# Optimization experiments

Measured on AMD Instinct MI355X. Metric: run time of the kernel, lower is better.

The kernel has to match this reference:

```python
import jax, jax.numpy as jnp
import numpy as np
import math

N, M = 512, 31
INP, EMB, ATT = 64, 64, 64
NUM_RELS = 200
SELF_LOOP_IDX = NUM_RELS  # index num_rels is the self-loop relation


def setup_inputs() -> dict:
    key = jax.random.key(0)
    ks = jax.random.split(key, 11)
    s_w = 1.0 / math.sqrt(EMB)
    return {
        "h": jax.random.normal(ks[0], (N, INP), jnp.float32),
        "msg": jax.random.normal(ks[1], (N, M, EMB), jnp.float32),
        "msg_type": jax.random.randint(ks[2], (N, M), 0, NUM_RELS, jnp.int32),
        "r_label_node": jax.random.randint(ks[3], (N,), 0, NUM_RELS, jnp.int32),
        "r_label_msg": jax.random.randint(ks[4], (N, M), 0, NUM_RELS, jnp.int32),
        "W_self": jax.random.normal(ks[5], (INP, EMB), jnp.float32) * s_w,
        "Q": jax.random.normal(ks[6], (NUM_RELS + 1, EMB, ATT), jnp.float32) * s_w,
        "K": jax.random.normal(ks[7], (NUM_RELS + 1, EMB, ATT), jnp.float32) * s_w,
        "V": jax.random.normal(ks[8], (NUM_RELS + 1, EMB, ATT), jnp.float32) * s_w,
        "ffn_w": jax.random.normal(ks[9], (ATT, EMB), jnp.float32) * s_w,
        "ffn_b": jnp.zeros((EMB,), jnp.float32),
    }


def reference(h, msg, msg_type, r_label_node, r_label_msg, W_self, Q, K, V, ffn_w, ffn_b):
    curr = h @ W_self                                        # [N, EMB]
    x = jnp.concatenate([curr[:, None, :], msg], axis=1)     # [N, M+1, EMB]
    qv_idx = jnp.concatenate([r_label_node[:, None], r_label_msg], axis=1)  # [N, M+1]
    self_col = jnp.full((x.shape[0], 1), SELF_LOOP_IDX, msg_type.dtype)
    k_idx = jnp.concatenate([self_col, msg_type], axis=1)    # [N, M+1]
    # relation-indexed per-token projection weights (irregular gather)
    q = jnp.einsum("nme,nmea->nma", x, Q[qv_idx])            # [N, M+1, ATT]
    k = jnp.einsum("nme,nmea->nma", x, K[k_idx])             # [N, M+1, ATT]
    v = jnp.einsum("nme,nmea->nma", x, V[qv_idx])            # [N, M+1, ATT]
    scores = jnp.einsum("nqa,nka->nqk", q, k) / math.sqrt(ATT)
    # NOTE: original code applies softmax over dim=1 (the query axis)
    att = jax.nn.softmax(scores, axis=1)                     # [N, M+1, M+1]
    pooled = jnp.einsum("nqk,nka->nqa", att, v)[:, 0]        # [N, ATT]
    return pooled @ ffn_w + ffn_b                            # [N, EMB]
```

## Files before the change

kernel.cpp:

```cpp
#include <hip/hip_runtime.h>
#include <math.h>

#define NN 512
#define MM 31
#define TT 32
#define EE 64
#define NREL 200
#define SELF_LOOP 200
#define QCAP 192
#define NT 6
#define WSTR 72
#define CPAD 32

typedef short  short8 __attribute__((ext_vector_type(8)));
typedef float  f32x4  __attribute__((ext_vector_type(4)));

__device__ __forceinline__ unsigned short f2bf(float f) {
    union { float f; unsigned int u; } a; a.f = f;
    unsigned int r = a.u + 0x7FFFu + ((a.u >> 16) & 1u);
    return (unsigned short)(r >> 16);
}

__global__ __launch_bounds__(64) void prep_scan_kernel(
    const float* __restrict__ h, const float* __restrict__ W_self,
    const float* __restrict__ K,
    const int* __restrict__ msg_type, const int* __restrict__ r_label_node,
    const int* __restrict__ r_label_msg,
    int* __restrict__ cnt_q, int* __restrict__ cnt_k,
    int* __restrict__ list_q, int* __restrict__ list_k,
    float* __restrict__ curr_all, float* __restrict__ k_all)
{
    const int n = blockIdx.x, a = threadIdx.x;

    if (a == 0) {
        int r = r_label_node[n];
        int p = atomicAdd(&cnt_q[r * CPAD], 1);
        if (p < QCAP) list_q[r * QCAP + p] = n * TT;
    }
    if (a < MM) {
        int j  = n * MM + a;
        int rl = r_label_msg[j];
        int p  = atomicAdd(&cnt_q[rl * CPAD], 1);
        if (p < QCAP) list_q[rl * QCAP + p] = n * TT + a + 1;
        int mt = msg_type[j];
        int p2 = atomicAdd(&cnt_k[mt * CPAD], 1);
        if (p2 < QCAP) list_k[mt * QCAP + p2] = n * TT + a + 1;
    }

    __shared__ float c_s[EE];
    const float* hrow = h + n * EE;
    float acc = 0.f;
#pragma unroll 8
    for (int e = 0; e < EE; ++e)
        acc = fmaf(hrow[e], W_self[e * EE + a], acc);
    curr_all[n * EE + a] = acc;
    c_s[a] = acc;
    __syncthreads();

    const float* K200 = K + (size_t)SELF_LOOP * EE * EE;
    float k0 = 0.f;
#pragma unroll 8
    for (int e = 0; e < EE; ++e)
        k0 = fmaf(c_s[e], K200[e * EE + a], k0);
    k_all[(size_t)n * TT * EE + a] = k0;
}

__global__ __launch_bounds__(256) void proj_tile_kernel(
    const float* __restrict__ curr_all, const float* __restrict__ msg,
    const float* __restrict__ Q, const float* __restrict__ K,
    const float* __restrict__ V,
    const int* __restrict__ cnt_q, const int* __restrict__ cnt_k,
    const int* __restrict__ list_q, const int* __restrict__ list_k,
    float* __restrict__ q_all, float* __restrict__ k_all,
    float* __restrict__ v_all)
{
    const int r    = blockIdx.x / NT;
    const int tile = blockIdx.x % NT;
    const int tid  = threadIdx.x;
    const int lane = tid & 63;
    const int wave = tid >> 6;
    const int col  = lane & 15;
    const int quad = lane >> 4;

    const int nq = min(cnt_q[r * CPAD], QCAP);
    const int nk = min(cnt_k[r * CPAD], QCAP);
    const int q0 = tile * 32;
    const bool do_q = q0 < nq;
    const bool do_k = q0 < nk;
    if (!do_q && !do_k) return;

    __shared__ unsigned short wq_s[EE * WSTR];
    __shared__ unsigned short wk_s[EE * WSTR];
    __shared__ unsigned short wv_s[EE * WSTR];
    __shared__ unsigned short x_s[64 * WSTR];
    __shared__ int tq_s[32], tk_s[32];

    {
        const int a = tid & 63, g = tid >> 6;
        if (do_q) {
            const float* Qp = Q + (size_t)r * EE * EE;
            const float* Vp = V + (size_t)r * EE * EE;
            unsigned short bq[16], bv[16];
#pragma unroll
            for (int j = 0; j < 16; ++j) {
                int e = g * 16 + j;
                bq[j] = f2bf(Qp[e * EE + a]);
                bv[j] = f2bf(Vp[e * EE + a]);
            }
            unsigned short* dq = &wq_s[a * WSTR + g * 16];
            unsigned short* dv = &wv_s[a * WSTR + g * 16];
            *(short8*)dq = *(short8*)&bq[0]; *(short8*)(dq + 8) = *(short8*)&bq[8];
            *(short8*)dv = *(short8*)&bv[0]; *(short8*)(dv + 8) = *(short8*)&bv[8];
        }
        if (do_k) {
            const float* Kp = K + (size_t)r * EE * EE;
            unsigned short bk[16];
#pragma unroll
            for (int j = 0; j < 16; ++j) {
                int e = g * 16 + j;
                bk[j] = f2bf(Kp[e * EE + a]);
            }
            unsigned short* dk = &wk_s[a * WSTR + g * 16];
            *(short8*)dk = *(short8*)&bk[0]; *(short8*)(dk + 8) = *(short8*)&bk[8];
        }
    }

    if (tid < 32) {
        tq_s[tid] = (do_q && q0 + tid < nq) ? list_q[r * QCAP + q0 + tid] : -1;
    } else if (tid < 64) {
        int i = tid - 32;
        tk_s[i] = (do_k && q0 + i < nk) ? list_k[r * QCAP + q0 + i] : -1;
    }

    {
        const int row = tid >> 2;
        const int fo  = (tid & 3) * 4;
        const bool qside = row < 32;
        const int li = qside ? (q0 + row) : (q0 + row - 32);
        const bool valid = qside ? (do_q && li < nq) : (do_k && li < nk);
        if (valid) {
            int token = qside ? list_q[r * QCAP + li] : list_k[r * QCAP + li];
            int n = token >> 5, t = token & 31;
            const float* src = (t == 0)
                ? (curr_all + n * EE)
                : (msg + ((size_t)n * MM + (t - 1)) * EE);
            float4 f0 = ((const float4*)src)[fo + 0];
            float4 f1 = ((const float4*)src)[fo + 1];
            float4 f2 = ((const float4*)src)[fo + 2];
            float4 f3 = ((const float4*)src)[fo + 3];
            unsigned short b[16] = {
                f2bf(f0.x), f2bf(f0.y), f2bf(f0.z), f2bf(f0.w),
                f2bf(f1.x), f2bf(f1.y), f2bf(f1.z), f2bf(f1.w),
                f2bf(f2.x), f2bf(f2.y), f2bf(f2.z), f2bf(f2.w),
                f2bf(f3.x), f2bf(f3.y), f2bf(f3.z), f2bf(f3.w) };
            unsigned short* d = &x_s[row * WSTR + fo * 4];
            *(short8*)d       = *(short8*)&b[0];
            *(short8*)(d + 8) = *(short8*)&b[8];
        }
    }
    __syncthreads();

    if (do_q) {
        const int mtile = wave & 1;
        const unsigned short* w_s = (wave >> 1) ? wv_s : wq_s;
        float* outp = (wave >> 1) ? v_all : q_all;
        const int m = mtile * 16 + col;
        f32x4 acc[4] = {{0,0,0,0},{0,0,0,0},{0,0,0,0},{0,0,0,0}};
#pragma unroll
        for (int kk = 0; kk < 2; ++kk) {
            short8 af = *(const short8*)&x_s[m * WSTR + kk * 32 + quad * 8];
#pragma unroll
            for (int nt = 0; nt < 4; ++nt) {
                short8 bf = *(const short8*)&w_s[(nt * 16 + col) * WSTR + kk * 32 + quad * 8];
                acc[nt] = __builtin_amdgcn_mfma_f32_16x16x32_bf16(af, bf, acc[nt], 0, 0, 0);
            }
        }
#pragma unroll
        for (int nt = 0; nt < 4; ++nt)
#pragma unroll
            for (int reg = 0; reg < 4; ++reg) {
                int rrow = mtile * 16 + quad * 4 + reg;
                int token = tq_s[rrow];
                if (token >= 0)
                    outp[(size_t)token * EE + nt * 16 + col] = acc[nt][reg];
            }
    }

    if (do_k) {
        const int mtile = wave & 1;
        const int nh = wave >> 1;
        const int m = 32 + mtile * 16 + col;
        f32x4 acc[2] = {{0,0,0,0},{0,0,0,0}};
#pragma unroll
        for (int kk = 0; kk < 2; ++kk) {
            short8 af = *(const short8*)&x_s[m * WSTR + kk * 32 + quad * 8];
#pragma unroll
            for (int j = 0; j < 2; ++j) {
                int nt = nh * 2 + j;
                short8 bf = *(const short8*)&wk_s[(nt * 16 + col) * WSTR + kk * 32 + quad * 8];
                acc[j] = __builtin_amdgcn_mfma_f32_16x16x32_bf16(af, bf, acc[j], 0, 0, 0);
            }
        }
#pragma unroll
        for (int j = 0; j < 2; ++j)
#pragma unroll
            for (int reg = 0; reg < 4; ++reg) {
                int rrow = mtile * 16 + quad * 4 + reg;
                int token = tk_s[rrow];
                if (token >= 0)
                    k_all[(size_t)token * EE + (nh * 2 + j) * 16 + col] = acc[j][reg];
            }
    }
}

__global__ __launch_bounds__(256) void attn_kernel(
    const float* __restrict__ q_all, const float* __restrict__ k_all,
    const float* __restrict__ v_all, const float* __restrict__ ffn_w,
    const float* __restrict__ ffn_b, float* __restrict__ out)
{
    const int n = blockIdx.x, tid = threadIdx.x;
    __shared__ float q_s[TT][68], k_s[TT][68], v_s[TT][68];
    __shared__ float s_s[TT][TT + 1];
    __shared__ float att0[TT];
    __shared__ float pooled[EE];

    {
        const float4* qg = (const float4*)(q_all + (size_t)n * TT * EE);
        const float4* kg = (const float4*)(k_all + (size_t)n * TT * EE);
        const float4* vg = (const float4*)(v_all + (size_t)n * TT * EE);
        for (int i = tid; i < TT * EE / 4; i += 256) {
            int row = i >> 4, c = i & 15;
            ((float4*)&q_s[row][0])[c] = qg[i];
            ((float4*)&k_s[row][0])[c] = kg[i];
            ((float4*)&v_s[row][0])[c] = vg[i];
        }
    }
    __syncthreads();

    {
        const int ki = tid & 31;
        for (int qi = tid >> 5; qi < TT; qi += 8) {
            const float4* qp = (const float4*)&q_s[qi][0];
            const float4* kp = (const float4*)&k_s[ki][0];
            float acc = 0.f;
            for (int e4 = 0; e4 < EE / 4; ++e4) {
                float4 a = qp[e4], b = kp[e4];
                acc += a.x * b.x + a.y * b.y + a.z * b.z + a.w * b.w;
            }
            s_s[qi][ki] = acc * 0.125f;
        }
    }
    __syncthreads();

    if (tid < TT) {
        float mx = -INFINITY;
        for (int qi = 0; qi < TT; ++qi) mx = fmaxf(mx, s_s[qi][tid]);
        float sum = 0.f;
        for (int qi = 0; qi < TT; ++qi) sum += __expf(s_s[qi][tid] - mx);
        att0[tid] = __expf(s_s[0][tid] - mx) / sum;
    }
    __syncthreads();

    if (tid < EE) {
        float acc = 0.f;
        for (int ki = 0; ki < TT; ++ki)
            acc = fmaf(att0[ki], v_s[ki][tid], acc);
        pooled[tid] = acc;
    }
    __syncthreads();

    if (tid < EE) {
        float acc = ffn_b[tid];
        for (int a = 0; a < EE; ++a)
            acc = fmaf(pooled[a], ffn_w[a * EE + tid], acc);
        out[n * EE + tid] = acc;
    }
}

extern "C" void kernel_launch(void* const* d_in, const int* in_sizes, int n_in,
                              void* d_out, int out_size, void* d_ws, size_t ws_size,
                              hipStream_t stream) {
    const float* h            = (const float*)d_in[0];
    const float* msg          = (const float*)d_in[1];
    const int*   msg_type     = (const int*)  d_in[2];
    const int*   r_label_node = (const int*)  d_in[3];
    const int*   r_label_msg  = (const int*)  d_in[4];
    const float* W_self       = (const float*)d_in[5];
    const float* Q            = (const float*)d_in[6];
    const float* K            = (const float*)d_in[7];
    const float* V            = (const float*)d_in[8];
    const float* ffn_w        = (const float*)d_in[9];
    const float* ffn_b        = (const float*)d_in[10];
    float*       out          = (float*)d_out;

    int* cnt_q  = (int*)d_ws;
    int* cnt_k  = cnt_q + NREL * CPAD;
    int* list_q = cnt_k + NREL * CPAD;
    int* list_k = list_q + NREL * QCAP;
    float* curr_all = (float*)(list_k + NREL * QCAP);
    float* q_all = curr_all + NN * EE;
    float* k_all = q_all + (size_t)NN * TT * EE;
    float* v_all = k_all + (size_t)NN * TT * EE;

    hipMemsetAsync(cnt_q, 0, 2 * NREL * CPAD * sizeof(int), stream);
    prep_scan_kernel<<<NN, 64, 0, stream>>>(h, W_self, K, msg_type,
                                            r_label_node, r_label_msg,
                                            cnt_q, cnt_k, list_q, list_k,
                                            curr_all, k_all);
    proj_tile_kernel<<<NREL * NT, 256, 0, stream>>>(curr_all, msg, Q, K, V,
                                                    cnt_q, cnt_k, list_q, list_k,
                                                    q_all, k_all, v_all);
    attn_kernel<<<NN, 256, 0, stream>>>(q_all, k_all, v_all, ffn_w, ffn_b, out);
}
```

Measured before the change: 109.4 us.

## Pre-convert and transpose Q/K/V weights to bf16 once in prep kernel

The prep kernel now gets extra blocks that convert each relation's Q, K and V matrix to bf16 and transpose it through shared memory into a workspace buffer. The projection tile kernel then loads these pre-transposed bf16 weights with vectorized 16-byte loads, instead of reading fp32 columns with strided access and converting them in each of up to six tiles per relation. This removes repeated conversion and uncoalesced weight reads from the projection stage. In exchange it converts all 201 matrices, including unused tiles, adds workspace traffic, and widens the prep kernel's blocks to 256 threads while only 64 do the node work.

```diff
diff --git a/kernel.cpp b/kernel.cpp
--- a/kernel.cpp
+++ b/kernel.cpp
@@ -6,6 +6,7 @@
 #define TT 32
 #define EE 64
 #define NREL 200
+#define NMAT 201
 #define SELF_LOOP 200
 #define QCAP 192
 #define NT 6
@@ -21,54 +22,97 @@
     return (unsigned short)(r >> 16);
 }
 
-__global__ __launch_bounds__(64) void prep_scan_kernel(
+__global__ __launch_bounds__(256) void prep_convert_kernel(
     const float* __restrict__ h, const float* __restrict__ W_self,
-    const float* __restrict__ K,
+    const float* __restrict__ Q, const float* __restrict__ K,
+    const float* __restrict__ V,
     const int* __restrict__ msg_type, const int* __restrict__ r_label_node,
     const int* __restrict__ r_label_msg,
     int* __restrict__ cnt_q, int* __restrict__ cnt_k,
     int* __restrict__ list_q, int* __restrict__ list_k,
+    unsigned short* __restrict__ wt_q, unsigned short* __restrict__ wt_k,
+    unsigned short* __restrict__ wt_v,
     float* __restrict__ curr_all, float* __restrict__ k_all)
 {
-    const int n = blockIdx.x, a = threadIdx.x;
-
-    if (a == 0) {
+    const int bid = blockIdx.x, tid = threadIdx.x;
+
+    if (bid < 3 * NMAT) {
+        const int r   = bid % NMAT;
+        const int mat = bid / NMAT;
+        const float* src = (mat == 0 ? Q : mat == 1 ? K : V) + (size_t)r * EE * EE;
+        unsigned short* dst = (mat == 0 ? wt_q : mat == 1 ? wt_k : wt_v)
+                              + (size_t)r * EE * EE;
+        __shared__ unsigned short t_s[EE * WSTR];
+
+        {
+            const int e = tid >> 2, aseg = (tid & 3) * 16;
+            const float4* s4 = (const float4*)(src + e * EE + aseg);
+            float4 f0 = s4[0], f1 = s4[1], f2 = s4[2], f3 = s4[3];
+            unsigned short b[16] = {
+                f2bf(f0.x), f2bf(f0.y), f2bf(f0.z), f2bf(f0.w),
+                f2bf(f1.x), f2bf(f1.y), f2bf(f1.z), f2bf(f1.w),
+                f2bf(f2.x), f2bf(f2.y), f2bf(f2.z), f2bf(f2.w),
+                f2bf(f3.x), f2bf(f3.y), f2bf(f3.z), f2bf(f3.w) };
+            unsigned short* d = &t_s[e * WSTR + aseg];
+            *(short8*)d = *(short8*)&b[0];
+            *(short8*)(d + 8) = *(short8*)&b[8];
+        }
+        __syncthreads();
+        {
+            const int a = tid >> 2, eseg = (tid & 3) * 16;
+            unsigned short o[16];
+#pragma unroll
+            for (int j = 0; j < 16; ++j)
+                o[j] = t_s[(eseg + j) * WSTR + a];
+            unsigned short* d = dst + a * EE + eseg;
+            *(short8*)d = *(short8*)&o[0];
+            *(short8*)(d + 8) = *(short8*)&o[8];
+        }
+        return;
+    }
+
+    const int n = bid - 3 * NMAT;
+
+    if (tid < MM) {
+        int j  = n * MM + tid;
+        int rl = r_label_msg[j];
+        int p  = atomicAdd(&cnt_q[rl * CPAD], 1);
+        if (p < QCAP) list_q[rl * QCAP + p] = n * TT + tid + 1;
+        int mt = msg_type[j];
+        int p2 = atomicAdd(&cnt_k[mt * CPAD], 1);
+        if (p2 < QCAP) list_k[mt * QCAP + p2] = n * TT + tid + 1;
+    } else if (tid == 63) {
         int r = r_label_node[n];
         int p = atomicAdd(&cnt_q[r * CPAD], 1);
         if (p < QCAP) list_q[r * QCAP + p] = n * TT;
     }
-    if (a < MM) {
-        int j  = n * MM + a;
-        int rl = r_label_msg[j];
-        int p  = atomicAdd(&cnt_q[rl * CPAD], 1);
-        if (p < QCAP) list_q[rl * QCAP + p] = n * TT + a + 1;
-        int mt = msg_type[j];
-        int p2 = atomicAdd(&cnt_k[mt * CPAD], 1);
-        if (p2 < QCAP) list_k[mt * QCAP + p2] = n * TT + a + 1;
-    }
 
     __shared__ float c_s[EE];
-    const float* hrow = h + n * EE;
-    float acc = 0.f;
+    if (tid < EE) {
+        const float* hrow = h + n * EE;
+        float acc = 0.f;
 #pragma unroll 8
-    for (int e = 0; e < EE; ++e)
-        acc = fmaf(hrow[e], W_self[e * EE + a], acc);
-    curr_all[n * EE + a] = acc;
-    c_s[a] = acc;
-    __syncthreads();
-
-    const float* K200 = K + (size_t)SELF_LOOP * EE * EE;
-    float k0 = 0.f;
+        for (int e = 0; e < EE; ++e)
+            acc = fmaf(hrow[e], W_self[e * EE + tid], acc);
+        curr_all[n * EE + tid] = acc;
+        c_s[tid] = acc;
+    }
+    __syncthreads();
+    if (tid < EE) {
+        const float* K200 = K + (size_t)SELF_LOOP * EE * EE;
+        float k0 = 0.f;
 #pragma unroll 8
-    for (int e = 0; e < EE; ++e)
-        k0 = fmaf(c_s[e], K200[e * EE + a], k0);
-    k_all[(size_t)n * TT * EE + a] = k0;
+        for (int e = 0; e < EE; ++e)
+            k0 = fmaf(c_s[e], K200[e * EE + tid], k0);
+        k_all[(size_t)n * TT * EE + tid] = k0;
+    }
 }
 
 __global__ __launch_bounds__(256) void proj_tile_kernel(
     const float* __restrict__ curr_all, const float* __restrict__ msg,
-    const float* __restrict__ Q, const float* __restrict__ K,
-    const float* __restrict__ V,
+    const unsigned short* __restrict__ wt_q,
+    const unsigned short* __restrict__ wt_k,
+    const unsigned short* __restrict__ wt_v,
     const int* __restrict__ cnt_q, const int* __restrict__ cnt_k,
     const int* __restrict__ list_q, const int* __restrict__ list_k,
     float* __restrict__ q_all, float* __restrict__ k_all,
@@ -96,32 +140,21 @@
     __shared__ int tq_s[32], tk_s[32];
 
     {
-        const int a = tid & 63, g = tid >> 6;
+        const int a = tid >> 2, seg = (tid & 3) * 16;
+        const size_t go = (size_t)r * EE * EE + a * EE + seg;
+        const int lo = a * WSTR + seg;
         if (do_q) {
-            const float* Qp = Q + (size_t)r * EE * EE;
-            const float* Vp = V + (size_t)r * EE * EE;
-            unsigned short bq[16], bv[16];
-#pragma unroll
-            for (int j = 0; j < 16; ++j) {
-                int e = g * 16 + j;
-                bq[j] = f2bf(Qp[e * EE + a]);
-                bv[j] = f2bf(Vp[e * EE + a]);
-            }
-            unsigned short* dq = &wq_s[a * WSTR + g * 16];
-            unsigned short* dv = &wv_s[a * WSTR + g * 16];
-            *(short8*)dq = *(short8*)&bq[0]; *(short8*)(dq + 8) = *(short8*)&bq[8];
-            *(short8*)dv = *(short8*)&bv[0]; *(short8*)(dv + 8) = *(short8*)&bv[8];
+            short8 w0 = *(const short8*)(wt_q + go);
+            short8 w1 = *(const short8*)(wt_q + go + 8);
+            *(short8*)&wq_s[lo] = w0; *(short8*)&wq_s[lo + 8] = w1;
+            short8 v0 = *(const short8*)(wt_v + go);
+            short8 v1 = *(const short8*)(wt_v + go + 8);
+            *(short8*)&wv_s[lo] = v0; *(short8*)&wv_s[lo + 8] = v1;
         }
         if (do_k) {
-            const float* Kp = K + (size_t)r * EE * EE;
-            unsigned short bk[16];
-#pragma unroll
-            for (int j = 0; j < 16; ++j) {
-                int e = g * 16 + j;
-                bk[j] = f2bf(Kp[e * EE + a]);
-            }
-            unsigned short* dk = &wk_s[a * WSTR + g * 16];
-            *(short8*)dk = *(short8*)&bk[0]; *(short8*)(dk + 8) = *(short8*)&bk[8];
+            short8 k0_ = *(const short8*)(wt_k + go);
+            short8 k1_ = *(const short8*)(wt_k + go + 8);
+            *(short8*)&wk_s[lo] = k0_; *(short8*)&wk_s[lo + 8] = k1_;
         }
     }
 
@@ -297,18 +330,20 @@
     int* cnt_k  = cnt_q + NREL * CPAD;
     int* list_q = cnt_k + NREL * CPAD;
     int* list_k = list_q + NREL * QCAP;
-    float* curr_all = (float*)(list_k + NREL * QCAP);
+    unsigned short* wt_q = (unsigned short*)(list_k + NREL * QCAP);
+    unsigned short* wt_k = wt_q + (size_t)NMAT * EE * EE;
+    unsigned short* wt_v = wt_k + (size_t)NMAT * EE * EE;
+    float* curr_all = (float*)(wt_v + (size_t)NMAT * EE * EE);
     float* q_all = curr_all + NN * EE;
     float* k_all = q_all + (size_t)NN * TT * EE;
     float* v_all = k_all + (size_t)NN * TT * EE;
 
     hipMemsetAsync(cnt_q, 0, 2 * NREL * CPAD * sizeof(int), stream);
-    prep_scan_kernel<<<NN, 64, 0, stream>>>(h, W_self, K, msg_type,
-                                            r_label_node, r_label_msg,
-                                            cnt_q, cnt_k, list_q, list_k,
-                                            curr_all, k_all);
-    proj_tile_kernel<<<NREL * NT, 256, 0, stream>>>(curr_all, msg, Q, K, V,
-                                                    cnt_q, cnt_k, list_q, list_k,
-                                                    q_all, k_all, v_all);
+    prep_convert_kernel<<<3 * NMAT + NN, 256, 0, stream>>>(
+        h, W_self, Q, K, V, msg_type, r_label_node, r_label_msg,
+        cnt_q, cnt_k, list_q, list_k, wt_q, wt_k, wt_v, curr_all, k_all);
+    proj_tile_kernel<<<NREL * NT, 256, 0, stream>>>(
+        curr_all, msg, wt_q, wt_k, wt_v, cnt_q, cnt_k, list_q, list_k,
+        q_all, k_all, v_all);
     attn_kernel<<<NN, 256, 0, stream>>>(q_all, k_all, v_all, ffn_w, ffn_b, out);
 }
```

Measured after the change: 108.7 us. Within noise of the previous version (-0.6%).
